# Optimization experiments

Hardware: AMD Instinct MI355X
Metric: run time of the kernel (lower is better)

Reference implementation:

```python
import math
import jax, jax.numpy as jnp
import numpy as np

B, L, DIM, H = 2, 2048, 1024, 16
D = DIM // H  # head_dim = 64
EPS = 1e-6


def setup_inputs() -> dict:
    key = jax.random.key(0)
    ks = jax.random.split(key, 5)
    s = 0.02
    return {
        "x": jax.random.normal(ks[0], (B, L, DIM), jnp.float32),
        "pe": jax.random.normal(ks[1], (B, 1, L, D // 2, 2, 2), jnp.float32),
        "w_qkv": jax.random.normal(ks[2], (DIM, 3 * DIM), jnp.float32) * s,
        "q_scale": jnp.ones((D,), jnp.float32),
        "k_scale": jnp.ones((D,), jnp.float32),
        "w_proj": jax.random.normal(ks[3], (DIM, DIM), jnp.float32) * s,
        "b_proj": jnp.zeros((DIM,), jnp.float32),
    }


def _rmsnorm(t, scale):
    # flax nnx.RMSNorm: x * rsqrt(mean(x^2) + eps) * scale, over last dim
    var = jnp.mean(jnp.square(t), axis=-1, keepdims=True)
    return t * jax.lax.rsqrt(var + EPS) * scale


def _apply_rope(t, pe):
    # t: [B,H,L,D]; pe: [B,1,L,D/2,2,2]
    t2 = t.reshape(*t.shape[:-1], D // 2, 1, 2)
    out = pe[..., 0] * t2[..., 0] + pe[..., 1] * t2[..., 1]  # [B,H,L,D/2,2]
    return out.reshape(t.shape)


def reference(x, pe, w_qkv, q_scale, k_scale, w_proj, b_proj):
    # fused QKV projection
    qkv = jnp.einsum('bld,de->ble', x, w_qkv)  # [B,L,3*DIM]
    qkv = qkv.reshape(B, L, 3, H, D).transpose(2, 0, 3, 1, 4)  # [3,B,H,L,D]
    q, k, v = qkv[0], qkv[1], qkv[2]
    # QK RMSNorm
    q = _rmsnorm(q, q_scale)
    k = _rmsnorm(k, k_scale)
    # RoPE via pe
    q = _apply_rope(q, pe)
    k = _apply_rope(k, pe)
    # scaled dot product attention
    scores = jnp.einsum('bhqd,bhkd->bhqk', q, k) / math.sqrt(D)
    attn = jax.nn.softmax(scores, axis=-1)
    o = jnp.einsum('bhqk,bhkd->bhqd', attn, v)  # [B,H,L,D]
    o = o.transpose(0, 2, 1, 3).reshape(B, L, DIM)  # B H L D -> B L (H D)
    # output projection
    return jnp.einsum('bld,de->ble', o, w_proj) + b_proj
```

## Files before the change

### kernel.cpp

```cpp
#include <hip/hip_runtime.h>
#include <math.h>

#define BB 2
#define LL 2048
#define DIMM 1024
#define HH 16
#define DD 64
#define QKV_N 3072

typedef unsigned short u16;
typedef unsigned int u32;
typedef __attribute__((ext_vector_type(8))) short short8;
typedef __attribute__((ext_vector_type(4))) float f32x4;

__device__ __forceinline__ float bf2f(u16 h) {
    unsigned u = ((unsigned)h) << 16;
    return __uint_as_float(u);
}
__device__ __forceinline__ u16 f2bf(float f) {
    unsigned u = __float_as_uint(f);
    u += 0x7fffu + ((u >> 16) & 1u);
    return (u16)(u >> 16);
}
__device__ __forceinline__ u32 pack_bf2(float lo, float hi) {
    u32 a = __float_as_uint(hi) + 0x8000u;
    u32 b = __float_as_uint(lo) + 0x8000u;
    return __builtin_amdgcn_perm(a, b, 0x07060302u);
}
__device__ __forceinline__ void gload16(const u16* g, u16* l) {
    __builtin_amdgcn_global_load_lds(
        (const __attribute__((address_space(1))) void*)g,
        (__attribute__((address_space(3))) void*)l, 16, 0, 0);
}

__global__ __launch_bounds__(256) void convx(
    const float* __restrict__ X, u16* __restrict__ Xb)
{
    int i = (blockIdx.x * 256 + threadIdx.x) * 8;
    float4 a = *(const float4*)&X[i];
    float4 b = *(const float4*)&X[i + 4];
    u16 t[8] = {f2bf(a.x), f2bf(a.y), f2bf(a.z), f2bf(a.w),
                f2bf(b.x), f2bf(b.y), f2bf(b.z), f2bf(b.w)};
    *(uint4*)&Xb[i] = *(uint4*)t;
}

__global__ __launch_bounds__(256) void convt(
    const float* __restrict__ W, u16* __restrict__ Wt, int K, int N)
{
    __shared__ u16 s[64][72];
    const int tid = threadIdx.x;
    const int k0 = blockIdx.x * 64, n0 = blockIdx.y * 64;
#pragma unroll
    for (int t = 0; t < 16; ++t) {
        int flat = t * 256 + tid;
        int kk = flat >> 6, nn = flat & 63;
        s[nn][kk] = f2bf(W[(size_t)(k0 + kk) * N + n0 + nn]);
    }
    __syncthreads();
#pragma unroll
    for (int t = 0; t < 2; ++t) {
        int chunk = t * 256 + tid;
        int nn = chunk >> 3, kc = chunk & 7;
        *(uint4*)&Wt[(size_t)(n0 + nn) * K + k0 + kc * 8] = *(uint4*)&s[nn][kc * 8];
    }
}

__global__ __launch_bounds__(256) void vtrans(
    const u16* __restrict__ qkv, u16* __restrict__ vt)
{
    __shared__ u16 s[64][72];
    const int tid = threadIdx.x;
    const int bh = blockIdx.y;
    const int b = bh >> 4, h = bh & 15;
    const int l0 = blockIdx.x * 64;
    const u16* vbase = qkv + (size_t)b * LL * QKV_N + 2048 + h * 64;
#pragma unroll
    for (int t = 0; t < 2; ++t) {
        int flat = t * 2048 + tid * 8;
        int l = flat >> 6, d = flat & 63;
        *(uint4*)&s[l][d] = *(const uint4*)&vbase[(size_t)(l0 + l) * QKV_N + d];
    }
    __syncthreads();
#pragma unroll
    for (int t = 0; t < 2; ++t) {
        int flat = t * 2048 + tid * 8;
        int d = flat >> 6, l = flat & 63;
        u16 tmp[8];
#pragma unroll
        for (int j = 0; j < 8; ++j) tmp[j] = s[l + j][d];
        *(uint4*)&vt[((size_t)bh * 64 + d) * LL + l0 + l] = *(uint4*)tmp;
    }
}

__global__ __launch_bounds__(256) void gemm_qkv(
    const u16* __restrict__ A, const u16* __restrict__ Bt,
    u16* __restrict__ C, const float* __restrict__ pe,
    const float* __restrict__ qs, const float* __restrict__ ks)
{
    __shared__ u16 sA[128 * 64];
    __shared__ u16 sB[128 * 64];

    const int tid = threadIdx.x;
    const int wave = tid >> 6, lane = tid & 63;
    const int mIdx = lane & 15, quad = lane >> 4;
    const int wr = wave >> 1, wc = wave & 1;
    const int m0 = blockIdx.y * 128, n0 = blockIdx.x * 128;
    const int N = QKV_N, K = DIMM;
    const int lr = lane >> 3, lc = lane & 7;

    f32x4 acc[4][4];
#pragma unroll
    for (int a = 0; a < 4; ++a)
#pragma unroll
        for (int b = 0; b < 4; ++b) acc[a][b] = (f32x4){0.f, 0.f, 0.f, 0.f};

    for (int k0 = 0; k0 < K; k0 += 64) {
#pragma unroll
        for (int j = 0; j < 4; ++j) {
            int r0 = 32 * wave + 8 * j + lr;
            int kc = 8 * (lc ^ (r0 & 7));
            gload16(&A[(size_t)(m0 + r0) * K + k0 + kc], &sA[(32 * wave + 8 * j) * 64]);
            gload16(&Bt[(size_t)(n0 + r0) * K + k0 + kc], &sB[(32 * wave + 8 * j) * 64]);
        }
        __syncthreads();
#pragma unroll
        for (int ks2 = 0; ks2 < 2; ++ks2) {
            short8 af[4], bfr[4];
#pragma unroll
            for (int mt = 0; mt < 4; ++mt) {
                int Ra = 64 * wr + 16 * mt + mIdx;
                af[mt] = *(const short8*)&sA[Ra * 64 + 8 * ((ks2 * 4 + quad) ^ (Ra & 7))];
            }
#pragma unroll
            for (int nt = 0; nt < 4; ++nt) {
                int Rb = 64 * wc + 16 * nt + mIdx;
                bfr[nt] = *(const short8*)&sB[Rb * 64 + 8 * ((ks2 * 4 + quad) ^ (Rb & 7))];
            }
#pragma unroll
            for (int mt = 0; mt < 4; ++mt)
#pragma unroll
                for (int nt = 0; nt < 4; ++nt)
                    acc[mt][nt] = __builtin_amdgcn_mfma_f32_16x16x32_bf16(
                        af[mt], bfr[nt], acc[mt][nt], 0, 0, 0);
        }
        __syncthreads();
    }

    if (n0 >= 2048) {
#pragma unroll
        for (int mt = 0; mt < 4; ++mt)
#pragma unroll
            for (int r = 0; r < 4; ++r) {
                int row = m0 + 64 * wr + 16 * mt + quad * 4 + r;
#pragma unroll
                for (int nt = 0; nt < 4; ++nt) {
                    int col = n0 + 64 * wc + 16 * nt + mIdx;
                    C[(size_t)row * N + col] = f2bf(acc[mt][nt][r]);
                }
            }
    } else {
        const float* scv = (n0 < 1024) ? qs : ks;
        const float pre = (n0 < 1024) ? 0.18033688011112042f : 1.0f;
        float scl[4];
#pragma unroll
        for (int nt = 0; nt < 4; ++nt) scl[nt] = scv[16 * nt + mIdx];

#pragma unroll
        for (int mt = 0; mt < 4; ++mt) {
#pragma unroll
            for (int r = 0; r < 4; ++r) {
                float s = 0.f;
#pragma unroll
                for (int nt = 0; nt < 4; ++nt) {
                    float a = acc[mt][nt][r];
                    s += a * a;
                }
                s += __shfl_xor(s, 1);
                s += __shfl_xor(s, 2);
                s += __shfl_xor(s, 4);
                s += __shfl_xor(s, 8);
                float rn = rsqrtf(s * (1.f / 64.f) + 1e-6f);
                int R = m0 + 64 * wr + 16 * mt + quad * 4 + r;
                size_t peo = (size_t)R * 128;
#pragma unroll
                for (int nt = 0; nt < 4; ++nt) {
                    float v = acc[mt][nt][r] * rn * scl[nt];
                    float pp = __shfl_xor(v, 1);
                    float2 pw = *(const float2*)&pe[peo + 2 * (16 * nt + mIdx)];
                    float e  = (mIdx & 1) ? pp : v;
                    float od = (mIdx & 1) ? v : pp;
                    C[(size_t)R * N + n0 + 64 * wc + 16 * nt + mIdx] =
                        f2bf((pw.x * e + pw.y * od) * pre);
                }
            }
        }
    }
}

__global__ __launch_bounds__(256) void gemm_proj(
    const u16* __restrict__ A, const u16* __restrict__ Bt,
    const float* __restrict__ bias, float* __restrict__ C)
{
    __shared__ u16 sA[64 * 64];
    __shared__ u16 sB[128 * 64];

    const int tid = threadIdx.x;
    const int wave = tid >> 6, lane = tid & 63;
    const int mIdx = lane & 15, quad = lane >> 4;
    const int wr = wave >> 1, wc = wave & 1;
    const int m0 = blockIdx.y * 64, n0 = blockIdx.x * 128;
    const int N = DIMM, K = DIMM;
    const int lr = lane >> 3, lc = lane & 7;

    f32x4 acc[2][4];
#pragma unroll
    for (int a = 0; a < 2; ++a)
#pragma unroll
        for (int b = 0; b < 4; ++b) acc[a][b] = (f32x4){0.f, 0.f, 0.f, 0.f};

    for (int k0 = 0; k0 < K; k0 += 64) {
#pragma unroll
        for (int j = 0; j < 2; ++j) {
            int r0 = 16 * wave + 8 * j + lr;
            int kc = 8 * (lc ^ (r0 & 7));
            gload16(&A[(size_t)(m0 + r0) * K + k0 + kc], &sA[(16 * wave + 8 * j) * 64]);
        }
#pragma unroll
        for (int j = 0; j < 4; ++j) {
            int r0 = 32 * wave + 8 * j + lr;
            int kc = 8 * (lc ^ (r0 & 7));
            gload16(&Bt[(size_t)(n0 + r0) * K + k0 + kc], &sB[(32 * wave + 8 * j) * 64]);
        }
        __syncthreads();
#pragma unroll
        for (int ks2 = 0; ks2 < 2; ++ks2) {
            short8 af[2], bfr[4];
#pragma unroll
            for (int mt = 0; mt < 2; ++mt) {
                int Ra = 32 * wr + 16 * mt + mIdx;
                af[mt] = *(const short8*)&sA[Ra * 64 + 8 * ((ks2 * 4 + quad) ^ (Ra & 7))];
            }
#pragma unroll
            for (int nt = 0; nt < 4; ++nt) {
                int Rb = 64 * wc + 16 * nt + mIdx;
                bfr[nt] = *(const short8*)&sB[Rb * 64 + 8 * ((ks2 * 4 + quad) ^ (Rb & 7))];
            }
#pragma unroll
            for (int mt = 0; mt < 2; ++mt)
#pragma unroll
                for (int nt = 0; nt < 4; ++nt)
                    acc[mt][nt] = __builtin_amdgcn_mfma_f32_16x16x32_bf16(
                        af[mt], bfr[nt], acc[mt][nt], 0, 0, 0);
        }
        __syncthreads();
    }

#pragma unroll
    for (int mt = 0; mt < 2; ++mt)
#pragma unroll
        for (int r = 0; r < 4; ++r) {
            int row = m0 + 32 * wr + 16 * mt + quad * 4 + r;
#pragma unroll
            for (int nt = 0; nt < 4; ++nt) {
                int col = n0 + 64 * wc + 16 * nt + mIdx;
                C[(size_t)row * N + col] = acc[mt][nt][r] + bias[col];
            }
        }
}

#define PR 72

__global__ __launch_bounds__(512, 4) void attn_mfma(
    const u16* __restrict__ qkv, const u16* __restrict__ vt, u16* __restrict__ o)
{
    __shared__ u16 sK[2][64 * PR];
    __shared__ u16 sVt[2][64 * PR];
    __shared__ u16 sP[128 * PR];

    const int tid = threadIdx.x;
    const int wave = tid >> 6;
    const int lane = tid & 63;
    const int mIdx = lane & 15;
    const int quad = lane >> 4;

    const int bh = blockIdx.x >> 4;
    const int qt = blockIdx.x & 15;
    const int b = bh >> 4, h = bh & 15;
    const int q0 = qt * 128;

    const u16* kbase = qkv + (size_t)b * LL * QKV_N + 1024 + h * 64;
    const u16* vbase = vt + (size_t)bh * 64 * LL;

    const u16* qrow = qkv + (size_t)b * LL * QKV_N + h * 64
                      + (size_t)(q0 + 16 * wave + mIdx) * QKV_N;
    short8 aq0 = *(const short8*)&qrow[quad * 8];
    short8 aq1 = *(const short8*)&qrow[32 + quad * 8];

    const int sr = tid >> 3;
    const int sc = (tid & 7) * 8;

    {
        uint4 kv4 = *(const uint4*)&kbase[(size_t)sr * QKV_N + sc];
        uint4 vv4 = *(const uint4*)&vbase[(size_t)sr * LL + sc];
        *(uint4*)&sK[0][sr * PR + sc] = kv4;
        *(uint4*)&sVt[0][sr * PR + sc] = vv4;
    }

    float lsum = 0.f;
    f32x4 Oacc[4];
#pragma unroll
    for (int nb = 0; nb < 4; ++nb) Oacc[nb] = (f32x4){0.f, 0.f, 0.f, 0.f};

    u16* sProw = &sP[(16 * wave + mIdx) * PR];

    for (int kt = 0; kt < 32; ++kt) {
        const int p = kt & 1;
        __syncthreads();

        if (kt + 1 < 32) {
            const int k0n = (kt + 1) * 64;
            uint4 kv4 = *(const uint4*)&kbase[(size_t)(k0n + sr) * QKV_N + sc];
            uint4 vv4 = *(const uint4*)&vbase[(size_t)sr * LL + k0n + sc];
            *(uint4*)&sK[p ^ 1][sr * PR + sc] = kv4;
            *(uint4*)&sVt[p ^ 1][sr * PR + sc] = vv4;
        }

#pragma unroll
        for (int nb = 0; nb < 4; ++nb) {
            short8 bk0 = *(const short8*)&sK[p][(16 * nb + mIdx) * PR + quad * 8];
            short8 bk1 = *(const short8*)&sK[p][(16 * nb + mIdx) * PR + 32 + quad * 8];
            f32x4 st = (f32x4){0.f, 0.f, 0.f, 0.f};
            st = __builtin_amdgcn_mfma_f32_16x16x32_bf16(bk0, aq0, st, 0, 0, 0);
            st = __builtin_amdgcn_mfma_f32_16x16x32_bf16(bk1, aq1, st, 0, 0, 0);

            float p0 = exp2f(st[0]), p1 = exp2f(st[1]);
            float p2 = exp2f(st[2]), p3 = exp2f(st[3]);
            lsum += (p0 + p1) + (p2 + p3);
            u32 w0 = pack_bf2(p0, p1);
            u32 w1 = pack_bf2(p2, p3);
            uint2 wpair; wpair.x = w0; wpair.y = w1;
            *(uint2*)&sProw[16 * nb + quad * 4] = wpair;
        }

        short8 pa0 = *(const short8*)&sProw[quad * 8];
        short8 pa1 = *(const short8*)&sProw[32 + quad * 8];
#pragma unroll
        for (int nb = 0; nb < 4; ++nb) {
            short8 bv0 = *(const short8*)&sVt[p][(16 * nb + mIdx) * PR + quad * 8];
            short8 bv1 = *(const short8*)&sVt[p][(16 * nb + mIdx) * PR + 32 + quad * 8];
            Oacc[nb] = __builtin_amdgcn_mfma_f32_16x16x32_bf16(pa0, bv0, Oacc[nb], 0, 0, 0);
            Oacc[nb] = __builtin_amdgcn_mfma_f32_16x16x32_bf16(pa1, bv1, Oacc[nb], 0, 0, 0);
        }
    }

    lsum += __shfl_xor(lsum, 16);
    lsum += __shfl_xor(lsum, 32);

#pragma unroll
    for (int r = 0; r < 4; ++r) {
        float lr = __shfl(lsum, quad * 4 + r);
        float linv = 1.f / lr;
        int rowg = b * LL + q0 + 16 * wave + quad * 4 + r;
#pragma unroll
        for (int nb = 0; nb < 4; ++nb) {
            o[(size_t)rowg * DIMM + h * 64 + 16 * nb + mIdx] = f2bf(Oacc[nb][r] * linv);
        }
    }
}

extern "C" void kernel_launch(void* const* d_in, const int* in_sizes, int n_in,
                              void* d_out, int out_size, void* d_ws, size_t ws_size,
                              hipStream_t stream) {
    const float* x       = (const float*)d_in[0];
    const float* pe      = (const float*)d_in[1];
    const float* w_qkv   = (const float*)d_in[2];
    const float* q_scale = (const float*)d_in[3];
    const float* k_scale = (const float*)d_in[4];
    const float* w_proj  = (const float*)d_in[5];
    const float* b_proj  = (const float*)d_in[6];
    float* out = (float*)d_out;

    char* ws = (char*)d_ws;
    u16* qkv    = (u16*)ws;  ws += (size_t)4096 * 3072 * 2;
    u16* o      = (u16*)ws;  ws += (size_t)4096 * 1024 * 2;
    u16* xb     = (u16*)ws;  ws += (size_t)4096 * 1024 * 2;
    u16* wqkvt  = (u16*)ws;  ws += (size_t)3072 * 1024 * 2;
    u16* wprojt = (u16*)ws;  ws += (size_t)1024 * 1024 * 2;
    u16* vtbuf  = (u16*)ws;  ws += (size_t)BB * HH * DD * LL * 2;

    convx<<<(4096 * 1024) / (256 * 8), 256, 0, stream>>>(x, xb);
    convt<<<dim3(1024 / 64, QKV_N / 64), 256, 0, stream>>>(w_qkv, wqkvt, DIMM, QKV_N);
    convt<<<dim3(1024 / 64, 1024 / 64), 256, 0, stream>>>(w_proj, wprojt, DIMM, DIMM);

    gemm_qkv<<<dim3(QKV_N / 128, (BB * LL) / 128), 256, 0, stream>>>(
        xb, wqkvt, qkv, pe, q_scale, k_scale);

    vtrans<<<dim3(LL / 64, BB * HH), 256, 0, stream>>>(qkv, vtbuf);

    attn_mfma<<<BB * HH * (LL / 128), 512, 0, stream>>>(qkv, vtbuf, o);

    gemm_proj<<<dim3(DIMM / 128, (BB * LL) / 64), 256, 0, stream>>>(
        o, wprojt, b_proj, out);
}
```

Baseline: 227.2 us.

## Fuse V transpose into QKV GEMM epilogue and restructure attention tiling

```diff
diff --git a/kernel.cpp b/kernel.cpp
--- a/kernel.cpp
+++ b/kernel.cpp
@@ -65,40 +65,14 @@
     }
 }
 
-__global__ __launch_bounds__(256) void vtrans(
-    const u16* __restrict__ qkv, u16* __restrict__ vt)
-{
-    __shared__ u16 s[64][72];
-    const int tid = threadIdx.x;
-    const int bh = blockIdx.y;
-    const int b = bh >> 4, h = bh & 15;
-    const int l0 = blockIdx.x * 64;
-    const u16* vbase = qkv + (size_t)b * LL * QKV_N + 2048 + h * 64;
-#pragma unroll
-    for (int t = 0; t < 2; ++t) {
-        int flat = t * 2048 + tid * 8;
-        int l = flat >> 6, d = flat & 63;
-        *(uint4*)&s[l][d] = *(const uint4*)&vbase[(size_t)(l0 + l) * QKV_N + d];
-    }
-    __syncthreads();
-#pragma unroll
-    for (int t = 0; t < 2; ++t) {
-        int flat = t * 2048 + tid * 8;
-        int d = flat >> 6, l = flat & 63;
-        u16 tmp[8];
-#pragma unroll
-        for (int j = 0; j < 8; ++j) tmp[j] = s[l + j][d];
-        *(uint4*)&vt[((size_t)bh * 64 + d) * LL + l0 + l] = *(uint4*)tmp;
-    }
-}
-
 __global__ __launch_bounds__(256) void gemm_qkv(
     const u16* __restrict__ A, const u16* __restrict__ Bt,
-    u16* __restrict__ C, const float* __restrict__ pe,
+    u16* __restrict__ C, u16* __restrict__ vt, const float* __restrict__ pe,
     const float* __restrict__ qs, const float* __restrict__ ks)
 {
-    __shared__ u16 sA[128 * 64];
-    __shared__ u16 sB[128 * 64];
+    __shared__ u16 smem[2 * 128 * 64];
+    u16* sA = smem;
+    u16* sB = smem + 128 * 64;
 
     const int tid = threadIdx.x;
     const int wave = tid >> 6, lane = tid & 63;
@@ -148,16 +122,30 @@
 
     if (n0 >= 2048) {
 #pragma unroll
-        for (int mt = 0; mt < 4; ++mt)
-#pragma unroll
-            for (int r = 0; r < 4; ++r) {
-                int row = m0 + 64 * wr + 16 * mt + quad * 4 + r;
-#pragma unroll
-                for (int nt = 0; nt < 4; ++nt) {
-                    int col = n0 + 64 * wc + 16 * nt + mIdx;
-                    C[(size_t)row * N + col] = f2bf(acc[mt][nt][r]);
-                }
-            }
+        for (int mt = 0; mt < 4; ++mt) {
+            int lofs = 64 * wr + 16 * mt + 4 * quad;
+#pragma unroll
+            for (int nt = 0; nt < 4; ++nt) {
+                int d = 64 * wc + 16 * nt + mIdx;
+                uint2 pr;
+                pr.x = pack_bf2(acc[mt][nt][0], acc[mt][nt][1]);
+                pr.y = pack_bf2(acc[mt][nt][2], acc[mt][nt][3]);
+                *(uint2*)&smem[d * 128 + (lofs ^ (8 * (d & 7)))] = pr;
+            }
+        }
+        __syncthreads();
+        {
+            const int d = tid >> 1, half = tid & 1;
+            const int hd = n0 - 2048 + d;
+            const int h = hd >> 6, dd = hd & 63;
+            const int b = m0 >> 11, l0 = m0 & 2047;
+            u16* dst = vt + ((size_t)((b * 16 + h) * 64 + dd)) * LL + l0 + half * 64;
+#pragma unroll
+            for (int c = 0; c < 8; ++c) {
+                int slot = (half * 64 + 8 * c) ^ (8 * (d & 7));
+                *(uint4*)&dst[8 * c] = *(const uint4*)&smem[d * 128 + slot];
+            }
+        }
     } else {
         const float* scv = (n0 < 1024) ? qs : ks;
         const float pre = (n0 < 1024) ? 0.18033688011112042f : 1.0f;
@@ -268,20 +256,21 @@
         }
 }
 
-#define PR 72
-
-__global__ __launch_bounds__(512, 4) void attn_mfma(
+#define PPR 68
+
+__global__ __launch_bounds__(256) void attn_mfma(
     const u16* __restrict__ qkv, const u16* __restrict__ vt, u16* __restrict__ o)
 {
-    __shared__ u16 sK[2][64 * PR];
-    __shared__ u16 sVt[2][64 * PR];
-    __shared__ u16 sP[128 * PR];
+    __shared__ u16 sK[64 * 64];
+    __shared__ u16 sVt[64 * 64];
+    __shared__ u16 sP[128 * PPR];
 
     const int tid = threadIdx.x;
     const int wave = tid >> 6;
     const int lane = tid & 63;
     const int mIdx = lane & 15;
     const int quad = lane >> 4;
+    const int lr = lane >> 3, lc = lane & 7;
 
     const int bh = blockIdx.x >> 4;
     const int qt = blockIdx.x & 15;
@@ -291,79 +280,103 @@
     const u16* kbase = qkv + (size_t)b * LL * QKV_N + 1024 + h * 64;
     const u16* vbase = vt + (size_t)bh * 64 * LL;
 
-    const u16* qrow = qkv + (size_t)b * LL * QKV_N + h * 64
-                      + (size_t)(q0 + 16 * wave + mIdx) * QKV_N;
-    short8 aq0 = *(const short8*)&qrow[quad * 8];
-    short8 aq1 = *(const short8*)&qrow[32 + quad * 8];
-
-    const int sr = tid >> 3;
-    const int sc = (tid & 7) * 8;
-
-    {
-        uint4 kv4 = *(const uint4*)&kbase[(size_t)sr * QKV_N + sc];
-        uint4 vv4 = *(const uint4*)&vbase[(size_t)sr * LL + sc];
-        *(uint4*)&sK[0][sr * PR + sc] = kv4;
-        *(uint4*)&sVt[0][sr * PR + sc] = vv4;
-    }
-
-    float lsum = 0.f;
-    f32x4 Oacc[4];
-#pragma unroll
-    for (int nb = 0; nb < 4; ++nb) Oacc[nb] = (f32x4){0.f, 0.f, 0.f, 0.f};
-
-    u16* sProw = &sP[(16 * wave + mIdx) * PR];
+    short8 aq[2][2];
+#pragma unroll
+    for (int s2 = 0; s2 < 2; ++s2) {
+        const u16* qrow = qkv
+            + ((size_t)(b * LL + q0 + 32 * wave + 16 * s2 + mIdx)) * QKV_N + h * 64;
+        aq[s2][0] = *(const short8*)&qrow[quad * 8];
+        aq[s2][1] = *(const short8*)&qrow[32 + quad * 8];
+    }
+
+    float lsum[2] = {0.f, 0.f};
+    f32x4 Oacc[2][4];
+#pragma unroll
+    for (int s2 = 0; s2 < 2; ++s2)
+#pragma unroll
+        for (int nb = 0; nb < 4; ++nb) Oacc[s2][nb] = (f32x4){0.f, 0.f, 0.f, 0.f};
+
+    u16* sProw[2] = { &sP[(32 * wave + mIdx) * PPR],
+                      &sP[(32 * wave + 16 + mIdx) * PPR] };
 
     for (int kt = 0; kt < 32; ++kt) {
-        const int p = kt & 1;
-        __syncthreads();
-
-        if (kt + 1 < 32) {
-            const int k0n = (kt + 1) * 64;
-            uint4 kv4 = *(const uint4*)&kbase[(size_t)(k0n + sr) * QKV_N + sc];
-            uint4 vv4 = *(const uint4*)&vbase[(size_t)sr * LL + k0n + sc];
-            *(uint4*)&sK[p ^ 1][sr * PR + sc] = kv4;
-            *(uint4*)&sVt[p ^ 1][sr * PR + sc] = vv4;
-        }
-
+        const int k0 = kt * 64;
+        __syncthreads();
+
+#pragma unroll
+        for (int j = 0; j < 2; ++j) {
+            int r0 = 16 * wave + 8 * j + lr;
+            int kc = 8 * (lc ^ (r0 & 7));
+            gload16(&kbase[(size_t)(k0 + r0) * QKV_N + kc], &sK[(16 * wave + 8 * j) * 64]);
+            gload16(&vbase[(size_t)r0 * LL + k0 + kc], &sVt[(16 * wave + 8 * j) * 64]);
+        }
+        __syncthreads();
+
+        f32x4 st[2][4];
 #pragma unroll
         for (int nb = 0; nb < 4; ++nb) {
-            short8 bk0 = *(const short8*)&sK[p][(16 * nb + mIdx) * PR + quad * 8];
-            short8 bk1 = *(const short8*)&sK[p][(16 * nb + mIdx) * PR + 32 + quad * 8];
-            f32x4 st = (f32x4){0.f, 0.f, 0.f, 0.f};
-            st = __builtin_amdgcn_mfma_f32_16x16x32_bf16(bk0, aq0, st, 0, 0, 0);
-            st = __builtin_amdgcn_mfma_f32_16x16x32_bf16(bk1, aq1, st, 0, 0, 0);
-
-            float p0 = exp2f(st[0]), p1 = exp2f(st[1]);
-            float p2 = exp2f(st[2]), p3 = exp2f(st[3]);
-            lsum += (p0 + p1) + (p2 + p3);
-            u32 w0 = pack_bf2(p0, p1);
-            u32 w1 = pack_bf2(p2, p3);
-            uint2 wpair; wpair.x = w0; wpair.y = w1;
-            *(uint2*)&sProw[16 * nb + quad * 4] = wpair;
-        }
-
-        short8 pa0 = *(const short8*)&sProw[quad * 8];
-        short8 pa1 = *(const short8*)&sProw[32 + quad * 8];
+            int rowK = 16 * nb + mIdx;
+            short8 bk0 = *(const short8*)&sK[rowK * 64 + 8 * (quad ^ (rowK & 7))];
+            short8 bk1 = *(const short8*)&sK[rowK * 64 + 8 * ((4 + quad) ^ (rowK & 7))];
+#pragma unroll
+            for (int s2 = 0; s2 < 2; ++s2) {
+                f32x4 a = (f32x4){0.f, 0.f, 0.f, 0.f};
+                a = __builtin_amdgcn_mfma_f32_16x16x32_bf16(bk0, aq[s2][0], a, 0, 0, 0);
+                a = __builtin_amdgcn_mfma_f32_16x16x32_bf16(bk1, aq[s2][1], a, 0, 0, 0);
+                st[s2][nb] = a;
+            }
+        }
+
+#pragma unroll
+        for (int s2 = 0; s2 < 2; ++s2) {
+#pragma unroll
+            for (int nb = 0; nb < 4; ++nb) {
+                float p0 = exp2f(st[s2][nb][0]), p1 = exp2f(st[s2][nb][1]);
+                float p2 = exp2f(st[s2][nb][2]), p3 = exp2f(st[s2][nb][3]);
+                lsum[s2] += (p0 + p1) + (p2 + p3);
+                uint2 pr;
+                pr.x = pack_bf2(p0, p1);
+                pr.y = pack_bf2(p2, p3);
+                *(uint2*)&sProw[s2][16 * nb + quad * 4] = pr;
+            }
+        }
+
+        short8 pa[2][2];
+#pragma unroll
+        for (int s2 = 0; s2 < 2; ++s2) {
+            pa[s2][0] = *(const short8*)&sProw[s2][quad * 8];
+            pa[s2][1] = *(const short8*)&sProw[s2][32 + quad * 8];
+        }
 #pragma unroll
         for (int nb = 0; nb < 4; ++nb) {
-            short8 bv0 = *(const short8*)&sVt[p][(16 * nb + mIdx) * PR + quad * 8];
-            short8 bv1 = *(const short8*)&sVt[p][(16 * nb + mIdx) * PR + 32 + quad * 8];
-            Oacc[nb] = __builtin_amdgcn_mfma_f32_16x16x32_bf16(pa0, bv0, Oacc[nb], 0, 0, 0);
-            Oacc[nb] = __builtin_amdgcn_mfma_f32_16x16x32_bf16(pa1, bv1, Oacc[nb], 0, 0, 0);
-        }
-    }
-
-    lsum += __shfl_xor(lsum, 16);
-    lsum += __shfl_xor(lsum, 32);
-
-#pragma unroll
-    for (int r = 0; r < 4; ++r) {
-        float lr = __shfl(lsum, quad * 4 + r);
-        float linv = 1.f / lr;
-        int rowg = b * LL + q0 + 16 * wave + quad * 4 + r;
-#pragma unroll
-        for (int nb = 0; nb < 4; ++nb) {
-            o[(size_t)rowg * DIMM + h * 64 + 16 * nb + mIdx] = f2bf(Oacc[nb][r] * linv);
+            int rowV = 16 * nb + mIdx;
+            short8 bv0 = *(const short8*)&sVt[rowV * 64 + 8 * (quad ^ (rowV & 7))];
+            short8 bv1 = *(const short8*)&sVt[rowV * 64 + 8 * ((4 + quad) ^ (rowV & 7))];
+#pragma unroll
+            for (int s2 = 0; s2 < 2; ++s2) {
+                Oacc[s2][nb] = __builtin_amdgcn_mfma_f32_16x16x32_bf16(
+                    pa[s2][0], bv0, Oacc[s2][nb], 0, 0, 0);
+                Oacc[s2][nb] = __builtin_amdgcn_mfma_f32_16x16x32_bf16(
+                    pa[s2][1], bv1, Oacc[s2][nb], 0, 0, 0);
+            }
+        }
+    }
+
+#pragma unroll
+    for (int s2 = 0; s2 < 2; ++s2) {
+        float ls = lsum[s2];
+        ls += __shfl_xor(ls, 16);
+        ls += __shfl_xor(ls, 32);
+#pragma unroll
+        for (int r = 0; r < 4; ++r) {
+            float lr2 = __shfl(ls, quad * 4 + r);
+            float linv = 1.f / lr2;
+            int rowg = b * LL + q0 + 32 * wave + 16 * s2 + quad * 4 + r;
+#pragma unroll
+            for (int nb = 0; nb < 4; ++nb) {
+                o[(size_t)rowg * DIMM + h * 64 + 16 * nb + mIdx] =
+                    f2bf(Oacc[s2][nb][r] * linv);
+            }
         }
     }
 }
@@ -393,11 +406,9 @@
     convt<<<dim3(1024 / 64, 1024 / 64), 256, 0, stream>>>(w_proj, wprojt, DIMM, DIMM);
 
     gemm_qkv<<<dim3(QKV_N / 128, (BB * LL) / 128), 256, 0, stream>>>(
-        xb, wqkvt, qkv, pe, q_scale, k_scale);
-
-    vtrans<<<dim3(LL / 64, BB * HH), 256, 0, stream>>>(qkv, vtbuf);
-
-    attn_mfma<<<BB * HH * (LL / 128), 512, 0, stream>>>(qkv, vtbuf, o);
+        xb, wqkvt, qkv, vtbuf, pe, q_scale, k_scale);
+
+    attn_mfma<<<BB * HH * (LL / 128), 256, 0, stream>>>(qkv, vtbuf, o);
 
     gemm_proj<<<dim3(DIMM / 128, (BB * LL) / 64), 256, 0, stream>>>(
         o, wprojt, b_proj, out);
```

New measurement: 249.3 us. 9.7% more time.
